# Optimization experiments

Hardware: AMD Instinct MI355X
Metric: run time of the kernel (lower is better)

Reference implementation:

```python
import jax, jax.numpy as jnp
import numpy as np


def setup_inputs() -> dict:
    key = jax.random.key(0)
    ks = jax.random.split(key, 6)
    N, E, F, H, HOP = 100000, 1600000, 128, 128, 3
    x = jax.random.normal(ks[0], (N, F), dtype=jnp.float32)
    edge_index = jax.random.randint(ks[1], (2, E), 0, N, dtype=jnp.int64)
    # per-hop weights, scaled like nn.Linear default init magnitude
    W1 = jax.random.normal(ks[2], (HOP, H, F), dtype=jnp.float32) * (1.0 / np.sqrt(F))
    W2 = jax.random.normal(ks[3], (HOP, H, H), dtype=jnp.float32) * (1.0 / np.sqrt(H))
    W3 = jax.random.normal(ks[4], (HOP, H, H), dtype=jnp.float32) * (1.0 / np.sqrt(H))
    W4 = jax.random.normal(ks[5], (HOP, H, 1), dtype=jnp.float32)
    return {"x": x, "edge_index": edge_index, "W1": W1, "W2": W2, "W3": W3, "W4": W4}


def reference(x, edge_index, W1, W2, W3, W4):
    N = x.shape[0]
    E = edge_index.shape[1]
    H = W1.shape[1]
    hop = W1.shape[0]
    row, col = edge_index[0], edge_index[1]
    edge_attr = jnp.ones((E, 1), dtype=x.dtype)  # as in original forward
    h = jnp.zeros((N, H), dtype=x.dtype)  # initial node_embedding
    for i in range(hop):
        node_feat = x @ W1[i].T                                   # [N,H]
        # gather neighbor embeddings then scatter-sum to destination nodes
        nbr_agg = jax.ops.segment_sum(h[col], row, num_segments=N)  # [N,H]
        edge_emb = jax.nn.relu(edge_attr @ W4[i].T)               # [E,H]
        edge_agg = jax.ops.segment_sum(edge_emb, row, num_segments=N)  # [N,H]
        h = jax.nn.relu(node_feat + nbr_agg @ W2[i].T + edge_agg @ W3[i].T)
        # dropout is identity in eval mode
    return h
```

## Files before the change

kernel.cpp:

```cpp
#include <hip/hip_runtime.h>

#define H 128
#define BCAP 18432

typedef __attribute__((ext_vector_type(8))) short bf16x8;
typedef __attribute__((ext_vector_type(4))) float f32x4;
typedef unsigned int uint;
typedef unsigned short ushort;

__device__ __forceinline__ ushort f2bf(float f) {
    uint u = __builtin_bit_cast(uint, f);
    uint r = u + 0x7FFFu + ((u >> 16) & 1u);
    return (ushort)(r >> 16);
}
__device__ __forceinline__ float bf_lo(uint u) {
    return __builtin_bit_cast(float, u << 16);
}
__device__ __forceinline__ float bf_hi(uint u) {
    return __builtin_bit_cast(float, u & 0xFFFF0000u);
}


__global__ void scatter_direct(const int* __restrict__ ei, int E, int NB,
                               int* __restrict__ gcnt, int2* __restrict__ ebuf) {
    __shared__ int cnt[1024];
    __shared__ int base[1024];
    int blk = blockIdx.x, t = threadIdx.x;
    for (int b = t; b < NB; b += 256) cnt[b] = 0;
    __syncthreads();
    int lo = blk << 12, hi = min(lo + 4096, E);
    for (int e = lo + t; e < hi; e += 256) atomicAdd(&cnt[ei[e] >> 10], 1);
    __syncthreads();
    for (int b = t; b < NB; b += 256) {
        int c = cnt[b];
        base[b] = c ? atomicAdd(&gcnt[b * 16], c) : 0;
        cnt[b] = 0;
    }
    __syncthreads();
    for (int e = lo + t; e < hi; e += 256) {
        int r = ei[e], c = ei[E + e];
        int b = r >> 10;
        int pos = base[b] + atomicAdd(&cnt[b], 1);
        if (pos < BCAP) ebuf[(size_t)b * BCAP + pos] = make_int2(r, c);
    }
}

__global__ __launch_bounds__(1024)
void bucket_csr2(const int2* __restrict__ ebuf, const int* __restrict__ gcnt,
                 int NB, int N, int* __restrict__ deg, int* __restrict__ off,
                 int* __restrict__ colss) {
    __shared__ int rcnt[1024], rloff[1024];
    int b = blockIdx.x, t = threadIdx.x;
    int rowbase = b << 10;
    int ebase = b * BCAP;
    int ne = min(gcnt[b * 16], BCAP);
    rcnt[t] = 0;
    __syncthreads();
    for (int e = t; e < ne; e += 1024) atomicAdd(&rcnt[ebuf[(size_t)ebase + e].x - rowbase], 1);
    __syncthreads();
    int v = rcnt[t];
    rloff[t] = v;
    __syncthreads();
    for (int d = 1; d < 1024; d <<= 1) {
        int u = (t >= d) ? rloff[t - d] : 0;
        __syncthreads();
        rloff[t] += u;
        __syncthreads();
    }
    int ex = rloff[t] - v;
    int row = rowbase + t;
    if (row < N) {
        deg[row] = v;
        off[row] = ebase + ex;
    }
    __syncthreads();
    rloff[t] = ex;
    rcnt[t] = 0;
    __syncthreads();
    for (int e = t; e < ne; e += 1024) {
        int2 rc = ebuf[(size_t)ebase + e];
        int lr = rc.x - rowbase;
        int pz = atomicAdd(&rcnt[lr], 1);
        colss[ebase + rloff[lr] + pz] = rc.y;
    }
}

__global__ void cvec_kernel(const float* __restrict__ W3, const float* __restrict__ W4,
                            float* __restrict__ cvec) {
    int i = blockIdx.x, k = threadIdx.x;
    const float* w3 = W3 + i * H * H + k * H;
    const float* w4 = W4 + i * H;
    float s = 0.f;
    for (int j = 0; j < H; ++j) s += w3[j] * fmaxf(w4[j], 0.f);
    cvec[i * H + k] = s;
}

__global__ void cast_bf16(const float* __restrict__ in, ushort* __restrict__ outp, int n8) {
    int i = blockIdx.x * blockDim.x + threadIdx.x;
    if (i >= n8) return;
    const float4* in4 = (const float4*)in;
    float4 a = in4[2 * i], b = in4[2 * i + 1];
    uint4 o;
    o.x = (uint)f2bf(a.x) | ((uint)f2bf(a.y) << 16);
    o.y = (uint)f2bf(a.z) | ((uint)f2bf(a.w) << 16);
    o.z = (uint)f2bf(b.x) | ((uint)f2bf(b.y) << 16);
    o.w = (uint)f2bf(b.z) | ((uint)f2bf(b.w) << 16);
    ((uint4*)outp)[i] = o;
}


template<int RELU, int OUT_BF16, int CAST0>
__global__ __launch_bounds__(256)
void gemm_pairs(const void* __restrict__ A0, const ushort* __restrict__ W0,
                const ushort* __restrict__ A1, const ushort* __restrict__ W1,
                int npairs, const int* __restrict__ deg, const float* __restrict__ cvec,
                void* __restrict__ Cout, ushort* __restrict__ xbout, int N)
{
    __shared__ uint4 A4[1024];
    __shared__ uint4 W4[1024];
    int t = threadIdx.x;
    int w = t >> 6, l = t & 63;
    int lg = l >> 4, lr = l & 15;
    int rowBase = blockIdx.x * 128;

    f32x4 acc[2][8];
#pragma unroll
    for (int rt = 0; rt < 2; ++rt)
#pragma unroll
        for (int ct = 0; ct < 8; ++ct) acc[rt][ct] = (f32x4){0.f, 0.f, 0.f, 0.f};

    for (int pr = 0; pr < npairs; ++pr) {
        const uint4* Ag = (const uint4*)(pr ? (const void*)A1 : A0);
        const uint4* Wg = (const uint4*)(pr ? W1 : W0);
        for (int kc = 0; kc < 2; ++kc) {
            if (pr || kc) __syncthreads();
#pragma unroll
            for (int it = 0; it < 4; ++it) {
                int idx = it * 256 + t;
                int r = idx >> 3, s = idx & 7;
                int gr = rowBase + r;
                uint4 v = make_uint4(0, 0, 0, 0);
                if (CAST0 && pr == 0) {
                    if (gr < N) {
                        const float4* xg = (const float4*)A0;
                        float4 a = xg[(size_t)gr * 32 + (kc * 8 + s) * 2];
                        float4 b = xg[(size_t)gr * 32 + (kc * 8 + s) * 2 + 1];
                        v.x = (uint)f2bf(a.x) | ((uint)f2bf(a.y) << 16);
                        v.y = (uint)f2bf(a.z) | ((uint)f2bf(a.w) << 16);
                        v.z = (uint)f2bf(b.x) | ((uint)f2bf(b.y) << 16);
                        v.w = (uint)f2bf(b.z) | ((uint)f2bf(b.w) << 16);
                        ((uint4*)xbout)[(size_t)gr * 16 + kc * 8 + s] = v;
                    }
                } else {
                    if (gr < N) v = Ag[(size_t)gr * 16 + kc * 8 + s];
                }
                A4[r * 8 + (s ^ (r & 7))] = v;
                W4[r * 8 + (s ^ (r & 7))] = Wg[r * 16 + kc * 8 + s];
            }
            __syncthreads();
#pragma unroll
            for (int kk = 0; kk < 2; ++kk) {
                int slot = kk * 4 + lg;
                bf16x8 af[2], bfr[8];
#pragma unroll
                for (int rt = 0; rt < 2; ++rt) {
                    int r = w * 32 + rt * 16 + lr;
                    af[rt] = *(const bf16x8*)&A4[r * 8 + (slot ^ (r & 7))];
                }
#pragma unroll
                for (int ct = 0; ct < 8; ++ct) {
                    int r = ct * 16 + lr;
                    bfr[ct] = *(const bf16x8*)&W4[r * 8 + (slot ^ (r & 7))];
                }
#pragma unroll
                for (int rt = 0; rt < 2; ++rt)
#pragma unroll
                    for (int ct = 0; ct < 8; ++ct)
                        acc[rt][ct] = __builtin_amdgcn_mfma_f32_16x16x32_bf16(
                            af[rt], bfr[ct], acc[rt][ct], 0, 0, 0);
            }
        }
    }

    float cv[8];
#pragma unroll
    for (int ct = 0; ct < 8; ++ct) cv[ct] = cvec[ct * 16 + lr];
#pragma unroll
    for (int rt = 0; rt < 2; ++rt) {
#pragma unroll
        for (int j = 0; j < 4; ++j) {
            int gr = rowBase + w * 32 + rt * 16 + lg * 4 + j;
            if (gr < N) {
                float d = (float)deg[gr];
#pragma unroll
                for (int ct = 0; ct < 8; ++ct) {
                    int gc = ct * 16 + lr;
                    float v = acc[rt][ct][j] + d * cv[ct];
                    if (RELU) v = fmaxf(v, 0.f);
                    if (OUT_BF16) ((ushort*)Cout)[(size_t)gr * H + gc] = f2bf(v);
                    else ((float*)Cout)[(size_t)gr * H + gc] = v;
                }
            }
        }
    }
}


__global__ void aggregate_sum(const ushort* __restrict__ hsrc,
                              const int* __restrict__ off, const int* __restrict__ deg,
                              const int* __restrict__ cols,
                              ushort* __restrict__ sdst, int N)
{
    int node = blockIdx.x * 4 + (threadIdx.x >> 6);
    if (node >= N) return;
    int l = threadIdx.x & 63;
    int half = l >> 5, lh = l & 31;
    int s = off[node];
    int d = deg[node];
    int e = s + d;
    const uint2* pu = (const uint2*)hsrc;
    float a0 = 0.f, a1 = 0.f, a2 = 0.f, a3 = 0.f;
    int i = s;
    if (d & 1) {
        if (half == 0) {
            uint2 v = pu[(size_t)cols[i] * 32 + lh];
            a0 += bf_lo(v.x); a1 += bf_hi(v.x);
            a2 += bf_lo(v.y); a3 += bf_hi(v.y);
        }
        ++i;
    }
    for (; i + 16 <= e; i += 16) {
        uint2 v0 = pu[(size_t)cols[i      + half] * 32 + lh];
        uint2 v1 = pu[(size_t)cols[i + 2  + half] * 32 + lh];
        uint2 v2 = pu[(size_t)cols[i + 4  + half] * 32 + lh];
        uint2 v3 = pu[(size_t)cols[i + 6  + half] * 32 + lh];
        uint2 v4 = pu[(size_t)cols[i + 8  + half] * 32 + lh];
        uint2 v5 = pu[(size_t)cols[i + 10 + half] * 32 + lh];
        uint2 v6 = pu[(size_t)cols[i + 12 + half] * 32 + lh];
        uint2 v7 = pu[(size_t)cols[i + 14 + half] * 32 + lh];
        a0 += bf_lo(v0.x) + bf_lo(v1.x) + bf_lo(v2.x) + bf_lo(v3.x)
            + bf_lo(v4.x) + bf_lo(v5.x) + bf_lo(v6.x) + bf_lo(v7.x);
        a1 += bf_hi(v0.x) + bf_hi(v1.x) + bf_hi(v2.x) + bf_hi(v3.x)
            + bf_hi(v4.x) + bf_hi(v5.x) + bf_hi(v6.x) + bf_hi(v7.x);
        a2 += bf_lo(v0.y) + bf_lo(v1.y) + bf_lo(v2.y) + bf_lo(v3.y)
            + bf_lo(v4.y) + bf_lo(v5.y) + bf_lo(v6.y) + bf_lo(v7.y);
        a3 += bf_hi(v0.y) + bf_hi(v1.y) + bf_hi(v2.y) + bf_hi(v3.y)
            + bf_hi(v4.y) + bf_hi(v5.y) + bf_hi(v6.y) + bf_hi(v7.y);
    }
    for (; i + 2 <= e; i += 2) {
        uint2 v = pu[(size_t)cols[i + half] * 32 + lh];
        a0 += bf_lo(v.x); a1 += bf_hi(v.x);
        a2 += bf_lo(v.y); a3 += bf_hi(v.y);
    }
    a0 += __shfl_xor(a0, 32);
    a1 += __shfl_xor(a1, 32);
    a2 += __shfl_xor(a2, 32);
    a3 += __shfl_xor(a3, 32);
    if (half == 0) {
        uint2 o;
        o.x = (uint)f2bf(a0) | ((uint)f2bf(a1) << 16);
        o.y = (uint)f2bf(a2) | ((uint)f2bf(a3) << 16);
        ((uint2*)sdst)[(size_t)node * 32 + lh] = o;
    }
}


extern "C" void kernel_launch(void* const* d_in, const int* in_sizes, int n_in,
                              void* d_out, int out_size, void* d_ws, size_t ws_size,
                              hipStream_t stream)
{
    const float* x  = (const float*)d_in[0];
    const int*   ei = (const int*)d_in[1];
    const float* W1 = (const float*)d_in[2];
    const float* W2 = (const float*)d_in[3];
    const float* W3 = (const float*)d_in[4];
    const float* W4 = (const float*)d_in[5];
    int N   = in_sizes[0] / H;
    int E   = in_sizes[1] / 2;
    int HOP = in_sizes[2] / (H * H);

    int NB   = (N + 1023) >> 10;
    int NBLK = (E + 4095) >> 12;

    char* ws = (char*)d_ws;
    int*   gcnt  = (int*)ws;
    int*   deg   = gcnt + NB * 16;
    int*   off   = deg + N;
    int*   colss = off + N;
    float* cvec  = (float*)(colss + (size_t)NB * BCAP);
    size_t fo = (((size_t)((char*)(cvec + HOP * H) - ws)) + 255) & ~(size_t)255;
    int2*  ebuf  = (int2*)(ws + fo);
    ushort* W1b  = (ushort*)(ebuf + (size_t)NB * BCAP);
    ushort* W2b  = W1b + (size_t)HOP * H * H;
    ushort* xb   = W2b + (size_t)HOP * H * H;
    ushort* h    = xb + (size_t)N * H;
    ushort* sagg = h + (size_t)N * H;

    hipMemsetAsync(gcnt, 0, sizeof(int) * NB * 16, stream);
    scatter_direct<<<NBLK, 256, 0, stream>>>(ei, E, NB, gcnt, ebuf);
    bucket_csr2<<<NB, 1024, 0, stream>>>(ebuf, gcnt, NB, N, deg, off, colss);

    cvec_kernel<<<HOP, H, 0, stream>>>(W3, W4, cvec);

    int nw8 = HOP * H * H / 8;
    cast_bf16<<<(nw8 + 255) / 256, 256, 0, stream>>>(W1, W1b, nw8);
    cast_bf16<<<(nw8 + 255) / 256, 256, 0, stream>>>(W2, W2b, nw8);

    int gblocks = (N + 127) / 128;
    float* out = (float*)d_out;

    if (HOP == 1) {
        gemm_pairs<1, 0, 1><<<gblocks, 256, 0, stream>>>(x, W1b, nullptr, nullptr, 1,
                                                         deg, cvec, out, xb, N);
        return;
    }
    gemm_pairs<1, 1, 1><<<gblocks, 256, 0, stream>>>(x, W1b, nullptr, nullptr, 1,
                                                     deg, cvec, h, xb, N);

    for (int i = 1; i < HOP; ++i) {
        int last = (i == HOP - 1);
        aggregate_sum<<<(N + 3) / 4, 256, 0, stream>>>(h, off, deg, colss, sagg, N);
        if (last)
            gemm_pairs<1, 0, 0><<<gblocks, 256, 0, stream>>>(xb, W1b + (size_t)i * H * H,
                                                             sagg, W2b + (size_t)i * H * H,
                                                             2, deg, cvec + i * H, out,
                                                             nullptr, N);
        else
            gemm_pairs<1, 1, 0><<<gblocks, 256, 0, stream>>>(xb, W1b + (size_t)i * H * H,
                                                             sagg, W2b + (size_t)i * H * H,
                                                             2, deg, cvec + i * H, h,
                                                             nullptr, N);
    }
}
```

Measured before the change: 274.2 us.

## Register-prefetch next GEMM K-chunk and simplify per-node gather to one row per wave

The GEMM kernel now loads the next K-chunk of A and W into registers while MFMAs run on the current shared-memory tile, then commits it to LDS after a barrier. This hides global-load latency behind compute at the cost of extra registers. Separately, the aggregation kernel has each wave lane read one uint (two bf16) per neighbor across the full 128-wide row, instead of splitting the wave into halves that each handle alternate neighbors. That removes the cross-half shuffle reduction and the odd-degree handling, but each load is narrower and fewer neighbors are in flight per iteration.

Result: slower. 286.0 us (+4.3%).

```diff
diff --git a/kernel.cpp b/kernel.cpp
--- a/kernel.cpp
+++ b/kernel.cpp
@@ -112,7 +112,7 @@
 template<int RELU, int OUT_BF16, int CAST0>
 __global__ __launch_bounds__(256)
 void gemm_pairs(const void* __restrict__ A0, const ushort* __restrict__ W0,
-                const ushort* __restrict__ A1, const ushort* __restrict__ W1,
+                const ushort* __restrict__ A1, const ushort* __restrict__ W1p,
                 int npairs, const int* __restrict__ deg, const float* __restrict__ cvec,
                 void* __restrict__ Cout, ushort* __restrict__ xbout, int N)
 {
@@ -129,56 +129,78 @@
 #pragma unroll
         for (int ct = 0; ct < 8; ++ct) acc[rt][ct] = (f32x4){0.f, 0.f, 0.f, 0.f};
 
-    for (int pr = 0; pr < npairs; ++pr) {
+    uint4 ar[4], wr[4];
+    int nc = npairs * 2;
+
+    auto stage = [&](int c) {
+        int pr = c >> 1, kc = c & 1;
         const uint4* Ag = (const uint4*)(pr ? (const void*)A1 : A0);
-        const uint4* Wg = (const uint4*)(pr ? W1 : W0);
-        for (int kc = 0; kc < 2; ++kc) {
-            if (pr || kc) __syncthreads();
-#pragma unroll
-            for (int it = 0; it < 4; ++it) {
-                int idx = it * 256 + t;
-                int r = idx >> 3, s = idx & 7;
-                int gr = rowBase + r;
-                uint4 v = make_uint4(0, 0, 0, 0);
-                if (CAST0 && pr == 0) {
-                    if (gr < N) {
-                        const float4* xg = (const float4*)A0;
-                        float4 a = xg[(size_t)gr * 32 + (kc * 8 + s) * 2];
-                        float4 b = xg[(size_t)gr * 32 + (kc * 8 + s) * 2 + 1];
-                        v.x = (uint)f2bf(a.x) | ((uint)f2bf(a.y) << 16);
-                        v.y = (uint)f2bf(a.z) | ((uint)f2bf(a.w) << 16);
-                        v.z = (uint)f2bf(b.x) | ((uint)f2bf(b.y) << 16);
-                        v.w = (uint)f2bf(b.z) | ((uint)f2bf(b.w) << 16);
-                        ((uint4*)xbout)[(size_t)gr * 16 + kc * 8 + s] = v;
-                    }
-                } else {
-                    if (gr < N) v = Ag[(size_t)gr * 16 + kc * 8 + s];
+        const uint4* Wg = (const uint4*)(pr ? W1p : W0);
+#pragma unroll
+        for (int it = 0; it < 4; ++it) {
+            int idx = it * 256 + t;
+            int r = idx >> 3, s = idx & 7;
+            int gr = rowBase + r;
+            uint4 v = make_uint4(0, 0, 0, 0);
+            if (CAST0 && pr == 0) {
+                if (gr < N) {
+                    const float4* xg = (const float4*)A0;
+                    float4 a = xg[(size_t)gr * 32 + (kc * 8 + s) * 2];
+                    float4 b = xg[(size_t)gr * 32 + (kc * 8 + s) * 2 + 1];
+                    v.x = (uint)f2bf(a.x) | ((uint)f2bf(a.y) << 16);
+                    v.y = (uint)f2bf(a.z) | ((uint)f2bf(a.w) << 16);
+                    v.z = (uint)f2bf(b.x) | ((uint)f2bf(b.y) << 16);
+                    v.w = (uint)f2bf(b.z) | ((uint)f2bf(b.w) << 16);
+                    ((uint4*)xbout)[(size_t)gr * 16 + kc * 8 + s] = v;
                 }
-                A4[r * 8 + (s ^ (r & 7))] = v;
-                W4[r * 8 + (s ^ (r & 7))] = Wg[r * 16 + kc * 8 + s];
+            } else {
+                if (gr < N) v = Ag[(size_t)gr * 16 + kc * 8 + s];
             }
+            ar[it] = v;
+            wr[it] = Wg[r * 16 + kc * 8 + s];
+        }
+    };
+    auto commit = [&]() {
+#pragma unroll
+        for (int it = 0; it < 4; ++it) {
+            int idx = it * 256 + t;
+            int r = idx >> 3, s = idx & 7;
+            A4[r * 8 + (s ^ (r & 7))] = ar[it];
+            W4[r * 8 + (s ^ (r & 7))] = wr[it];
+        }
+    };
+
+    stage(0);
+    commit();
+    __syncthreads();
+
+    for (int c = 0; c < nc; ++c) {
+        if (c + 1 < nc) stage(c + 1);
+#pragma unroll
+        for (int kk = 0; kk < 2; ++kk) {
+            int slot = kk * 4 + lg;
+            bf16x8 af[2], bfr[8];
+#pragma unroll
+            for (int rt = 0; rt < 2; ++rt) {
+                int r = w * 32 + rt * 16 + lr;
+                af[rt] = *(const bf16x8*)&A4[r * 8 + (slot ^ (r & 7))];
+            }
+#pragma unroll
+            for (int ct = 0; ct < 8; ++ct) {
+                int r = ct * 16 + lr;
+                bfr[ct] = *(const bf16x8*)&W4[r * 8 + (slot ^ (r & 7))];
+            }
+#pragma unroll
+            for (int rt = 0; rt < 2; ++rt)
+#pragma unroll
+                for (int ct = 0; ct < 8; ++ct)
+                    acc[rt][ct] = __builtin_amdgcn_mfma_f32_16x16x32_bf16(
+                        af[rt], bfr[ct], acc[rt][ct], 0, 0, 0);
+        }
+        __syncthreads();
+        if (c + 1 < nc) {
+            commit();
             __syncthreads();
-#pragma unroll
-            for (int kk = 0; kk < 2; ++kk) {
-                int slot = kk * 4 + lg;
-                bf16x8 af[2], bfr[8];
-#pragma unroll
-                for (int rt = 0; rt < 2; ++rt) {
-                    int r = w * 32 + rt * 16 + lr;
-                    af[rt] = *(const bf16x8*)&A4[r * 8 + (slot ^ (r & 7))];
-                }
-#pragma unroll
-                for (int ct = 0; ct < 8; ++ct) {
-                    int r = ct * 16 + lr;
-                    bfr[ct] = *(const bf16x8*)&W4[r * 8 + (slot ^ (r & 7))];
-                }
-#pragma unroll
-                for (int rt = 0; rt < 2; ++rt)
-#pragma unroll
-                    for (int ct = 0; ct < 8; ++ct)
-                        acc[rt][ct] = __builtin_amdgcn_mfma_f32_16x16x32_bf16(
-                            af[rt], bfr[ct], acc[rt][ct], 0, 0, 0);
-            }
         }
     }
 
@@ -214,54 +236,38 @@
     int node = blockIdx.x * 4 + (threadIdx.x >> 6);
     if (node >= N) return;
     int l = threadIdx.x & 63;
-    int half = l >> 5, lh = l & 31;
-    int s = off[node];
-    int d = deg[node];
-    int e = s + d;
-    const uint2* pu = (const uint2*)hsrc;
-    float a0 = 0.f, a1 = 0.f, a2 = 0.f, a3 = 0.f;
+    int s = off[node], e = s + deg[node];
+    const uint* pu = (const uint*)hsrc;
+    float ax = 0.f, ay = 0.f;
     int i = s;
-    if (d & 1) {
-        if (half == 0) {
-            uint2 v = pu[(size_t)cols[i] * 32 + lh];
-            a0 += bf_lo(v.x); a1 += bf_hi(v.x);
-            a2 += bf_lo(v.y); a3 += bf_hi(v.y);
-        }
-        ++i;
-    }
-    for (; i + 16 <= e; i += 16) {
-        uint2 v0 = pu[(size_t)cols[i      + half] * 32 + lh];
-        uint2 v1 = pu[(size_t)cols[i + 2  + half] * 32 + lh];
-        uint2 v2 = pu[(size_t)cols[i + 4  + half] * 32 + lh];
-        uint2 v3 = pu[(size_t)cols[i + 6  + half] * 32 + lh];
-        uint2 v4 = pu[(size_t)cols[i + 8  + half] * 32 + lh];
-        uint2 v5 = pu[(size_t)cols[i + 10 + half] * 32 + lh];
-        uint2 v6 = pu[(size_t)cols[i + 12 + half] * 32 + lh];
-        uint2 v7 = pu[(size_t)cols[i + 14 + half] * 32 + lh];
-        a0 += bf_lo(v0.x) + bf_lo(v1.x) + bf_lo(v2.x) + bf_lo(v3.x)
-            + bf_lo(v4.x) + bf_lo(v5.x) + bf_lo(v6.x) + bf_lo(v7.x);
-        a1 += bf_hi(v0.x) + bf_hi(v1.x) + bf_hi(v2.x) + bf_hi(v3.x)
-            + bf_hi(v4.x) + bf_hi(v5.x) + bf_hi(v6.x) + bf_hi(v7.x);
-        a2 += bf_lo(v0.y) + bf_lo(v1.y) + bf_lo(v2.y) + bf_lo(v3.y)
-            + bf_lo(v4.y) + bf_lo(v5.y) + bf_lo(v6.y) + bf_lo(v7.y);
-        a3 += bf_hi(v0.y) + bf_hi(v1.y) + bf_hi(v2.y) + bf_hi(v3.y)
-            + bf_hi(v4.y) + bf_hi(v5.y) + bf_hi(v6.y) + bf_hi(v7.y);
-    }
-    for (; i + 2 <= e; i += 2) {
-        uint2 v = pu[(size_t)cols[i + half] * 32 + lh];
-        a0 += bf_lo(v.x); a1 += bf_hi(v.x);
-        a2 += bf_lo(v.y); a3 += bf_hi(v.y);
-    }
-    a0 += __shfl_xor(a0, 32);
-    a1 += __shfl_xor(a1, 32);
-    a2 += __shfl_xor(a2, 32);
-    a3 += __shfl_xor(a3, 32);
-    if (half == 0) {
-        uint2 o;
-        o.x = (uint)f2bf(a0) | ((uint)f2bf(a1) << 16);
-        o.y = (uint)f2bf(a2) | ((uint)f2bf(a3) << 16);
-        ((uint2*)sdst)[(size_t)node * 32 + lh] = o;
-    }
+    for (; i + 8 <= e; i += 8) {
+        uint v0 = pu[(size_t)cols[i]     * 64 + l];
+        uint v1 = pu[(size_t)cols[i + 1] * 64 + l];
+        uint v2 = pu[(size_t)cols[i + 2] * 64 + l];
+        uint v3 = pu[(size_t)cols[i + 3] * 64 + l];
+        uint v4 = pu[(size_t)cols[i + 4] * 64 + l];
+        uint v5 = pu[(size_t)cols[i + 5] * 64 + l];
+        uint v6 = pu[(size_t)cols[i + 6] * 64 + l];
+        uint v7 = pu[(size_t)cols[i + 7] * 64 + l];
+        ax += bf_lo(v0) + bf_lo(v1) + bf_lo(v2) + bf_lo(v3)
+            + bf_lo(v4) + bf_lo(v5) + bf_lo(v6) + bf_lo(v7);
+        ay += bf_hi(v0) + bf_hi(v1) + bf_hi(v2) + bf_hi(v3)
+            + bf_hi(v4) + bf_hi(v5) + bf_hi(v6) + bf_hi(v7);
+    }
+    for (; i + 4 <= e; i += 4) {
+        uint v0 = pu[(size_t)cols[i]     * 64 + l];
+        uint v1 = pu[(size_t)cols[i + 1] * 64 + l];
+        uint v2 = pu[(size_t)cols[i + 2] * 64 + l];
+        uint v3 = pu[(size_t)cols[i + 3] * 64 + l];
+        ax += bf_lo(v0) + bf_lo(v1) + bf_lo(v2) + bf_lo(v3);
+        ay += bf_hi(v0) + bf_hi(v1) + bf_hi(v2) + bf_hi(v3);
+    }
+    for (; i < e; ++i) {
+        uint v = pu[(size_t)cols[i] * 64 + l];
+        ax += bf_lo(v);
+        ay += bf_hi(v);
+    }
+    ((uint*)sdst)[(size_t)node * 64 + l] = (uint)f2bf(ax) | ((uint)f2bf(ay) << 16);
 }
 
 
```
